# Optimization experiments

Hardware: AMD Instinct MI355X
Metric: run time of the kernel (lower is better)

Reference implementation:

```python
import jax, jax.numpy as jnp
import numpy as np

GAMMA, RHO, OMEGA = 0.7, 2.0, 0.5
EPS = 1e-6


def setup_inputs() -> dict:
    key = jax.random.key(0)
    S, T, N = 64, 256, 1024
    ks = jax.random.split(key, 7)
    x0 = jax.random.normal(ks[0], (N, 1), dtype=jnp.float32)
    # strictly increasing interaction times so dt > 0
    t = jnp.cumsum(jax.random.uniform(ks[1], (S, T), dtype=jnp.float32) + 0.1, axis=1)
    speed = jax.random.uniform(ks[2], (S, 1, 1, 1), dtype=jnp.float32) + 0.1
    vola = jax.random.uniform(ks[3], (S, 1, 1, 1), dtype=jnp.float32) + 0.1
    adj = (jax.random.uniform(ks[4], (N, N)) < 32.0 / N).astype(jnp.float32)
    noise = jax.random.normal(ks[5], (S, T - 1, N, 1), dtype=jnp.float32)
    items = jax.random.randint(ks[6], (S, T), 0, N)
    return {"x0": x0, "t": t, "speed": speed, "vola": vola,
            "adj": adj, "noise": noise, "items": items}


def _simulate(x0, t, speed, vola, adj, noise, items):
    S, T = t.shape
    N = x0.shape[0]
    dt = jnp.diff(t, axis=1)[:, :, None, None]                     # [S,T-1,1,1]
    # OU std: sqrt(vola^2 * (1 - exp(-2*speed*dt)) / (2*speed + 1e-6))
    scale = jnp.sqrt(vola * vola * (1.0 - jnp.exp(-2.0 * speed * dt))
                     / (2.0 * speed + 1e-6))                       # [S,T-1,1,1]
    noisy = noise * scale                                          # [S,T-1,N,1]

    adj_t = adj.T
    in_deg = adj_t.sum(axis=1)[None, :, None]                      # [1,N,1]
    has_in = in_deg > 0

    seq = jnp.arange(S)
    feat0 = jnp.zeros((S, N, 3), jnp.float32)
    feat0 = feat0.at[seq, items[:, 0], 0].add(1.0)
    feat0 = feat0.at[seq, items[:, 0], 2].add(1.0)
    x_init = jnp.broadcast_to(x0[None], (S, N, 1)).astype(jnp.float32)
    sp = speed[:, 0]                                               # [S,1,1]

    def step(carry, inp):
        x_prev, feat = carry
        dt_i, noisy_i, item_i = inp                                # [S,1,1],[S,N,1],[S]
        agg = jnp.einsum('mn,snk->smk', adj_t, x_prev)             # neighbor sum
        empower = jnp.where(has_in, GAMMA * agg / (in_deg + 1e-7), 0.0)
        stable = (feat[..., 1:2] / (feat[..., 0:1] + EPS)) ** RHO
        level = OMEGA * empower + (1.0 - OMEGA) * stable
        e = jnp.exp(-sp * dt_i)
        x_i = x_prev * e + (1.0 - e) * level + noisy_i
        cur_perf = jax.nn.sigmoid(x_i[seq, item_i, 0])
        success = (cur_perf >= 0.5).astype(jnp.float32)
        feat = feat.at[seq, item_i, 0].add(1.0)
        feat = feat.at[seq, item_i, 1].add(success)
        return (x_i, feat), x_i

    xs = (jnp.moveaxis(dt, 1, 0), jnp.moveaxis(noisy, 1, 0), items[:, 1:].T)
    (_, _), ys = jax.lax.scan(step, (x_init, feat0), xs)
    x = jnp.concatenate([x_init[:, None], jnp.moveaxis(ys, 0, 1)], axis=1)  # [S,T,N,1]
    return x


def reference(x0, t, speed, vola, adj, noise, items):
    return _simulate(x0, t, speed, vola, adj, noise, items)
```

## Files before the change

kernel.cpp:

```cpp
#include <hip/hip_runtime.h>

#define NN 1024
#define TT 256
#define MAXDEG 96

typedef unsigned short u16;


__device__ __forceinline__ int bofsB(int v) {
    int h = (v >> 5) & 31;
    return 1024 + ((v & ~31) | ((v & 31) ^ h));
}
__device__ __forceinline__ int bofsC(int v) {
    int h = (v >> 5) & 31;
    return 2048 + ((v & ~31) | ((v & 31) ^ ((13 * h + 5) & 31)));
}

__global__ __launch_bounds__(64) void k1_count(const float* __restrict__ adj,
                                               int* __restrict__ cnt_part)
{
    int tid = blockIdx.x * 64 + threadIdx.x;
    int chunk = tid >> 10;
    int n = tid & 1023;
    int c = 0;
    for (int j = 0; j < 64; ++j)
        c += (adj[(chunk * 64 + j) * NN + n] != 0.0f) ? 1 : 0;
    cnt_part[chunk * NN + n] = c;
}

__global__ __launch_bounds__(256) void k2_totals(const int* __restrict__ cnt_part,
                                                 int* __restrict__ deg,
                                                 int* __restrict__ pdeg)
{
    int n = blockIdx.x * 256 + threadIdx.x;
    int tot = 0;
    for (int c = 0; c < 16; ++c) tot += cnt_part[c * NN + n];
    deg[n] = tot;
    int cap = tot < MAXDEG ? tot : MAXDEG;
    int pd = (cap + 15) & ~7;
    if (pd < 16) pd = 16;
    if (pd > MAXDEG) pd = MAXDEG;
    pdeg[n] = pd;
}

__global__ __launch_bounds__(256) void k3_rank(const int* __restrict__ pdeg,
                                               int* __restrict__ rank_of,
                                               int* __restrict__ node_of)
{
    int n = blockIdx.x * 256 + threadIdx.x;
    int my = pdeg[n];
    int r = 0;
    for (int m = 0; m < NN; ++m) {
        int pm = pdeg[m];
        r += (pm > my) || (pm == my && m < n);
    }
    rank_of[n] = r;
    node_of[r] = n;
}

__global__ __launch_bounds__(64) void k4_fill(const float* __restrict__ adj,
                                              const int* __restrict__ cnt_part,
                                              u16* __restrict__ nbrC)
{
    int tid = blockIdx.x * 64 + threadIdx.x;
    int chunk = tid >> 10;
    int n = tid & 1023;
    int pos = 0;
    for (int c = 0; c < chunk; ++c) pos += cnt_part[c * NN + n];
    for (int j = 0; j < 64; ++j) {
        int m = chunk * 64 + j;
        if (adj[m * NN + n] != 0.0f) {
            if (pos < MAXDEG) nbrC[n * MAXDEG + pos] = (u16)m;
            ++pos;
        }
    }
}

__device__ __forceinline__ int cnt_res(int pd, int res) {
    return (pd > res) ? (((pd - 1 - res) >> 5) + 1) : 0;
}

__global__ __launch_bounds__(64) void k5_sched(const u16* __restrict__ nbrC,
                                               const int* __restrict__ deg,
                                               const int* __restrict__ pdeg,
                                               const int* __restrict__ rank_of,
                                               u16* __restrict__ nbr8,
                                               int* __restrict__ ngrp_r,
                                               float* __restrict__ invd_r)
{
    __shared__ int freec[32][64];
    const int tl = threadIdx.x;
    const int n  = blockIdx.x * 64 + tl;
    const int r  = rank_of[n];
    const int l  = r & 63;
    const int dg = deg[n];
    const int cap = dg < MAXDEG ? dg : MAXDEG;
    const int pd = pdeg[n];

    for (int res = 0; res < 32; ++res)
        freec[res][tl] = cnt_res(pd, res);

    for (int k = 0; k < pd; ++k) {
        int word = 3072 + ((l + k) & 31);
        nbr8[((k >> 3) << 13) + (r << 3) + (k & 7)] = (u16)(word * 4);
    }

    for (int j = 0; j < cap; ++j) {
        int v = rank_of[nbrC[n * MAXDEG + j]];
        int b0 = v & 31;
        int h  = (v >> 5) & 31;
        int b1 = b0 ^ h;
        int b2 = b0 ^ ((13 * h + 5) & 31);
        int res0 = (b0 - l) & 31;
        int res1 = (b1 - l) & 31;
        int res2 = (b2 - l) & 31;
        int kslot, word;
        int f0 = freec[res0][tl];
        if (f0 > 0) {
            kslot = res0 + 32 * (cnt_res(pd, res0) - f0);
            freec[res0][tl] = f0 - 1;
            word = v;
        } else {
            int f1 = freec[res1][tl];
            if (f1 > 0) {
                kslot = res1 + 32 * (cnt_res(pd, res1) - f1);
                freec[res1][tl] = f1 - 1;
                word = bofsB(v);
            } else {
                int f2 = freec[res2][tl];
                if (f2 > 0) {
                    kslot = res2 + 32 * (cnt_res(pd, res2) - f2);
                    freec[res2][tl] = f2 - 1;
                    word = bofsC(v);
                } else {
                    kslot = -1; word = v;
                    for (int res = 0; res < 32; ++res) {
                        int f = freec[res][tl];
                        if (f > 0) {
                            kslot = res + 32 * (cnt_res(pd, res) - f);
                            freec[res][tl] = f - 1;
                            break;
                        }
                    }
                }
            }
        }
        if (kslot >= 0)
            nbr8[((kslot >> 3) << 13) + (r << 3) + (kslot & 7)] = (u16)(word * 4);
    }
    ngrp_r[r] = pd >> 3;
    invd_r[r] = 0.35f / ((float)dg + 1e-7f);
}

#define LDS_BARRIER() asm volatile("s_waitcnt lgkmcnt(0)\n\ts_barrier" ::: "memory")

__global__ __launch_bounds__(1024) void sim_kernel(
    const float* __restrict__ x0, const float* __restrict__ t,
    const float* __restrict__ speed, const float* __restrict__ vola,
    const float* __restrict__ noise, const int* __restrict__ items,
    const u16* __restrict__ nbr8, const int* __restrict__ node_of,
    const int* __restrict__ rank_of,
    const int* __restrict__ ngrp_r, const float* __restrict__ invd_r,
    float* __restrict__ out)
{
    __shared__ float xb[2][3104];
    __shared__ float4 cst[TT - 1];

    const int s   = blockIdx.x;
    const int tid = threadIdx.x;

    const float sp = speed[s];
    const float vo = vola[s];

    if (tid < TT - 1) {
        float t0 = t[s * TT + tid], t1 = t[s * TT + tid + 1];
        float dt = t1 - t0;
        float e  = expf(-sp * dt);
        float sc = vo * sqrtf((1.0f - e * e) / (2.0f * sp + 1e-6f));
        int   it = items[s * TT + tid + 1];
        cst[tid] = make_float4(e, sc, __int_as_float(it), 0.0f);
    }

    const int   m     = node_of[tid];
    const int   r_out = rank_of[tid];
    const int   wB    = bofsB(tid);
    const int   wC    = bofsC(tid);

    const float x0m = x0[m];
    xb[0][tid] = x0m;
    xb[0][wB]  = x0m;
    xb[0][wC]  = x0m;
    if (tid < 32) { xb[0][3072 + tid] = 0.0f; xb[1][3072 + tid] = 0.0f; }

    float* __restrict__ outp = out + (size_t)s * TT * NN + tid;
    outp[0] = x0[tid];

    const int   ng   = ngrp_r[tid];
    const float invd = invd_r[tid];
    const int   item0 = items[s * TT];
    float a_f = (m == item0) ? 1.0f : 0.0f;
    float s_f = 0.0f;

    const float* __restrict__ nzm = noise + (size_t)s * (TT - 1) * NN + m;
    float nzA = nzm[0];
    float nzB = nzm[NN];

    const uint4* __restrict__ nb = (const uint4*)nbr8 + tid;
    uint4 q0  = nb[0];
    uint4 q1  = nb[1024];
    uint4 q2  = nb[2048];
    uint4 q3  = nb[3072];
    uint4 q4  = nb[4096];
    uint4 q5  = nb[5120];
    uint4 q6  = nb[6144];
    uint4 q7  = nb[7168];
    uint4 q8  = nb[8192];
    uint4 q9  = nb[9216];
    uint4 q10 = nb[10240];
    uint4 q11 = nb[11264];

    __syncthreads();

    float x_own = x0m;

#define G8(V)                                                   \
    acc += *(const float*)(xc + ((V).x & 0xFFFFu));             \
    acc += *(const float*)(xc + ((V).x >> 16));                 \
    acc += *(const float*)(xc + ((V).y & 0xFFFFu));             \
    acc += *(const float*)(xc + ((V).y >> 16));                 \
    acc += *(const float*)(xc + ((V).z & 0xFFFFu));             \
    acc += *(const float*)(xc + ((V).z >> 16));                 \
    acc += *(const float*)(xc + ((V).w & 0xFFFFu));             \
    acc += *(const float*)(xc + ((V).w >> 16));

    for (int i = 0; i < TT - 1; ++i) {
        const float* __restrict__ src = xb[i & 1];
        float* __restrict__ dst       = xb[(i + 1) & 1];
        const float4 c = cst[i];

        int ipre = (i + 2 < TT - 1) ? (i + 2) : (TT - 2);
        float nz_new = nzm[(size_t)ipre * NN];

        float xi_lin = src[r_out];

        float acc = 0.0f;
        const char* xc = (const char*)src;
        G8(q0); G8(q1);
        if (ng > 2) { G8(q2);
        if (ng > 3) { G8(q3);
        if (ng > 4) { G8(q4);
        if (ng > 5) { G8(q5);
        if (ng > 6) { G8(q6);
        if (ng > 7) { G8(q7);
        if (ng > 8) { G8(q8);
        if (ng > 9) { G8(q9);
        if (ng > 10){ G8(q10);
        if (ng > 11){ G8(q11); } } } } } } } } } }

        float nz = nzA * c.y;
        float r  = s_f / (a_f + 1e-6f);
        float level = fmaf(acc, invd, 0.5f * r * r);
        float xn = fmaf(x_own, c.x, fmaf(1.0f - c.x, level, nz));

        dst[tid] = xn;
        dst[wB]  = xn;
        dst[wC]  = xn;
        if (i) outp[(size_t)i * NN] = xi_lin;

        if (m == __float_as_int(c.z)) {
            a_f += 1.0f;
            s_f += (xn >= 0.0f) ? 1.0f : 0.0f;
        }
        x_own = xn;
        nzA = nzB; nzB = nz_new;
        LDS_BARRIER();
    }
#undef G8

    outp[(size_t)(TT - 1) * NN] = xb[1][r_out];
}

extern "C" void kernel_launch(void* const* d_in, const int* in_sizes, int n_in,
                              void* d_out, int out_size, void* d_ws, size_t ws_size,
                              hipStream_t stream)
{
    const float* x0    = (const float*)d_in[0];
    const float* t     = (const float*)d_in[1];
    const float* speed = (const float*)d_in[2];
    const float* vola  = (const float*)d_in[3];
    const float* adj   = (const float*)d_in[4];
    const float* noise = (const float*)d_in[5];
    const int*   items = (const int*)d_in[6];
    float* out = (float*)d_out;

    char* ws = (char*)d_ws;
    int*   cnt_part = (int*)ws;
    int*   deg      = (int*)(ws + 65536);
    int*   pdeg     = (int*)(ws + 65536 + 4096);
    int*   rank_of  = (int*)(ws + 65536 + 8192);
    int*   node_of  = (int*)(ws + 65536 + 12288);
    int*   ngrp_r   = (int*)(ws + 65536 + 16384);
    float* invd_r   = (float*)(ws + 65536 + 20480);
    u16*   nbrC     = (u16*)(ws + 65536 + 24576);
    u16*   nbr8     = (u16*)(ws + 65536 + 24576 + 196608);

    k1_count<<<256, 64, 0, stream>>>(adj, cnt_part);
    k2_totals<<<4, 256, 0, stream>>>(cnt_part, deg, pdeg);
    k3_rank<<<4, 256, 0, stream>>>(pdeg, rank_of, node_of);
    k4_fill<<<256, 64, 0, stream>>>(adj, cnt_part, nbrC);
    k5_sched<<<16, 64, 0, stream>>>(nbrC, deg, pdeg, rank_of, nbr8, ngrp_r, invd_r);
    sim_kernel<<<64, 1024, 0, stream>>>(x0, t, speed, vola, noise, items,
                                        nbr8, node_of, rank_of, ngrp_r, invd_r, out);
}
```

Measured before the change: 454.1 us.

## Balance bank-residue slot choice and trim neighbor groups in schedule kernel

The scheduler now picks among the three bank-aliased copies by whichever residue class has the most free slots, instead of always taking the first available. It records the highest slot actually filled and sets the per-row group count from it, so the simulation loop can skip trailing groups that hold only padding. The padding fill is written as packed 16-byte stores, and the kernel runs with 256-thread blocks. The aim is fewer LDS bank conflicts and fewer gather iterations per step in the main simulation. In exchange, the placement heuristic changes and group counts now depend on a minimum of two groups.

```diff
diff --git a/kernel.cpp b/kernel.cpp
--- a/kernel.cpp
+++ b/kernel.cpp
@@ -14,6 +14,9 @@
 __device__ __forceinline__ int bofsC(int v) {
     int h = (v >> 5) & 31;
     return 2048 + ((v & ~31) | ((v & 31) ^ ((13 * h + 5) & 31)));
+}
+__device__ __forceinline__ int cnt_res(int pd, int res) {
+    return (pd > res) ? (((pd - 1 - res) >> 5) + 1) : 0;
 }
 
 __global__ __launch_bounds__(64) void k1_count(const float* __restrict__ adj,
@@ -76,11 +79,7 @@
     }
 }
 
-__device__ __forceinline__ int cnt_res(int pd, int res) {
-    return (pd > res) ? (((pd - 1 - res) >> 5) + 1) : 0;
-}
-
-__global__ __launch_bounds__(64) void k5_sched(const u16* __restrict__ nbrC,
+__global__ __launch_bounds__(256) void k5_sched(const u16* __restrict__ nbrC,
                                                const int* __restrict__ deg,
                                                const int* __restrict__ pdeg,
                                                const int* __restrict__ rank_of,
@@ -88,9 +87,9 @@
                                                int* __restrict__ ngrp_r,
                                                float* __restrict__ invd_r)
 {
-    __shared__ int freec[32][64];
+    __shared__ int freec[32][256];
     const int tl = threadIdx.x;
-    const int n  = blockIdx.x * 64 + tl;
+    const int n  = blockIdx.x * 256 + tl;
     const int r  = rank_of[n];
     const int l  = r & 63;
     const int dg = deg[n];
@@ -100,11 +99,24 @@
     for (int res = 0; res < 32; ++res)
         freec[res][tl] = cnt_res(pd, res);
 
-    for (int k = 0; k < pd; ++k) {
-        int word = 3072 + ((l + k) & 31);
-        nbr8[((k >> 3) << 13) + (r << 3) + (k & 7)] = (u16)(word * 4);
-    }
-
+    for (int g = 0; g < (pd >> 3); ++g) {
+        uint4 pk;
+        unsigned w0 = (unsigned)((3072 + ((l + g * 8 + 0) & 31)) * 4);
+        unsigned w1 = (unsigned)((3072 + ((l + g * 8 + 1) & 31)) * 4);
+        unsigned w2 = (unsigned)((3072 + ((l + g * 8 + 2) & 31)) * 4);
+        unsigned w3 = (unsigned)((3072 + ((l + g * 8 + 3) & 31)) * 4);
+        unsigned w4 = (unsigned)((3072 + ((l + g * 8 + 4) & 31)) * 4);
+        unsigned w5 = (unsigned)((3072 + ((l + g * 8 + 5) & 31)) * 4);
+        unsigned w6 = (unsigned)((3072 + ((l + g * 8 + 6) & 31)) * 4);
+        unsigned w7 = (unsigned)((3072 + ((l + g * 8 + 7) & 31)) * 4);
+        pk.x = w0 | (w1 << 16);
+        pk.y = w2 | (w3 << 16);
+        pk.z = w4 | (w5 << 16);
+        pk.w = w6 | (w7 << 16);
+        *(uint4*)(nbr8 + (g << 13) + (r << 3)) = pk;
+    }
+
+    int maxk = 15;
     for (int j = 0; j < cap; ++j) {
         int v = rank_of[nbrC[n * MAXDEG + j]];
         int b0 = v & 31;
@@ -114,41 +126,39 @@
         int res0 = (b0 - l) & 31;
         int res1 = (b1 - l) & 31;
         int res2 = (b2 - l) & 31;
-        int kslot, word;
         int f0 = freec[res0][tl];
-        if (f0 > 0) {
+        int f1 = freec[res1][tl];
+        int f2 = freec[res2][tl];
+        int kslot = -1, word = v;
+        if (f0 > 0 && f0 >= f1 && f0 >= f2) {
             kslot = res0 + 32 * (cnt_res(pd, res0) - f0);
             freec[res0][tl] = f0 - 1;
             word = v;
+        } else if (f1 > 0 && f1 >= f2) {
+            kslot = res1 + 32 * (cnt_res(pd, res1) - f1);
+            freec[res1][tl] = f1 - 1;
+            word = bofsB(v);
+        } else if (f2 > 0) {
+            kslot = res2 + 32 * (cnt_res(pd, res2) - f2);
+            freec[res2][tl] = f2 - 1;
+            word = bofsC(v);
         } else {
-            int f1 = freec[res1][tl];
-            if (f1 > 0) {
-                kslot = res1 + 32 * (cnt_res(pd, res1) - f1);
-                freec[res1][tl] = f1 - 1;
-                word = bofsB(v);
-            } else {
-                int f2 = freec[res2][tl];
-                if (f2 > 0) {
-                    kslot = res2 + 32 * (cnt_res(pd, res2) - f2);
-                    freec[res2][tl] = f2 - 1;
-                    word = bofsC(v);
-                } else {
-                    kslot = -1; word = v;
-                    for (int res = 0; res < 32; ++res) {
-                        int f = freec[res][tl];
-                        if (f > 0) {
-                            kslot = res + 32 * (cnt_res(pd, res) - f);
-                            freec[res][tl] = f - 1;
-                            break;
-                        }
-                    }
+            for (int res = 0; res < 32; ++res) {
+                int f = freec[res][tl];
+                if (f > 0) {
+                    kslot = res + 32 * (cnt_res(pd, res) - f);
+                    freec[res][tl] = f - 1;
+                    word = v;
+                    break;
                 }
             }
         }
-        if (kslot >= 0)
+        if (kslot >= 0) {
             nbr8[((kslot >> 3) << 13) + (r << 3) + (kslot & 7)] = (u16)(word * 4);
-    }
-    ngrp_r[r] = pd >> 3;
+            if (kslot > maxk) maxk = kslot;
+        }
+    }
+    ngrp_r[r] = (maxk >> 3) + 1;
     invd_r[r] = 0.35f / ((float)dg + 1e-7f);
 }
 
@@ -308,7 +318,7 @@
     k2_totals<<<4, 256, 0, stream>>>(cnt_part, deg, pdeg);
     k3_rank<<<4, 256, 0, stream>>>(pdeg, rank_of, node_of);
     k4_fill<<<256, 64, 0, stream>>>(adj, cnt_part, nbrC);
-    k5_sched<<<16, 64, 0, stream>>>(nbrC, deg, pdeg, rank_of, nbr8, ngrp_r, invd_r);
+    k5_sched<<<4, 256, 0, stream>>>(nbrC, deg, pdeg, rank_of, nbr8, ngrp_r, invd_r);
     sim_kernel<<<64, 1024, 0, stream>>>(x0, t, speed, vola, noise, items,
                                         nbr8, node_of, rank_of, ngrp_r, invd_r, out);
 }
```

Measured after the change: 443.0 us. 2.4% less time.
